# Optimization experiments

Measured on AMD Instinct MI355X. Metric: run time of the kernel, lower is better.

Reference implementation:

```python
import jax, jax.numpy as jnp
import numpy as np

D = 768
N_HEADS = 12
HEAD_DIM = 64
INNER = N_HEADS * HEAD_DIM
SCALE = HEAD_DIM ** -0.5
EPS = 1e-5


def setup_inputs() -> dict:
    key = jax.random.key(0)
    ks = jax.random.split(key, 7)
    s = 0.02
    return {
        "x": jax.random.normal(ks[0], (2, 2048, D), dtype=jnp.float32),
        "Wq": jax.random.normal(ks[1], (D, INNER), dtype=jnp.float32) * s,
        "Wk": jax.random.normal(ks[2], (D, INNER), dtype=jnp.float32) * s,
        "Wv": jax.random.normal(ks[3], (D, INNER), dtype=jnp.float32) * s,
        "Wo": jax.random.normal(ks[4], (INNER, D), dtype=jnp.float32) * s,
        "bo": jnp.zeros((D,), dtype=jnp.float32),
        "gamma": jnp.ones((D,), dtype=jnp.float32),
        "beta": jnp.zeros((D,), dtype=jnp.float32),
    }


def _layernorm(x, gamma, beta):
    mu = jnp.mean(x, axis=-1, keepdims=True)
    var = jnp.var(x, axis=-1, keepdims=True)
    return (x - mu) * jax.lax.rsqrt(var + EPS) * gamma + beta


def reference(x, Wq, Wk, Wv, Wo, bo, gamma, beta):
    b, n, _ = x.shape
    h = _layernorm(x, gamma, beta)
    # project and split heads: [b, n, inner] -> [b, h, n, d]
    def split(t):
        return t.reshape(b, n, N_HEADS, HEAD_DIM).transpose(0, 2, 1, 3)
    Q = split(h @ Wq)
    K = split(h @ Wk)
    V = split(h @ Wv)
    # NOTE: module applies softmax first, THEN multiplies probs by scale
    attn = jnp.einsum('bhid,bhjd->bhij', Q, K)
    attn = jax.nn.softmax(attn, axis=-1) * SCALE
    vals = jnp.einsum('bhij,bhjd->bhid', attn, V)
    vals = vals.transpose(0, 2, 1, 3).reshape(b, n, INNER)
    out = vals @ Wo + bo
    return x + out
```

## Files before the change

kernel.cpp:

```cpp
#include <hip/hip_runtime.h>
#include <stdint.h>

typedef __bf16 bf16;
typedef __bf16 bf16x8 __attribute__((ext_vector_type(8)));
typedef float  f32x4  __attribute__((ext_vector_type(4)));
typedef unsigned short u16x4 __attribute__((ext_vector_type(4)));
typedef unsigned int   u32x4v __attribute__((ext_vector_type(4)));

#define SEQ   2048
#define DM    768
#define NH    12
#define HD    64
#define ATT_SCALE 0.125f
#define LOG2E 1.44269504f
#define LN_EPS 1e-5f

__device__ __forceinline__ void gload16(const void* g, void* l) {
  __builtin_amdgcn_global_load_lds((const __attribute__((address_space(1))) void*)g,
                                   (__attribute__((address_space(3))) void*)l,
                                   16, 0, 0);
}

__global__ __launch_bounds__(256) void prep_kernel(
    const float* __restrict__ x, const float* __restrict__ gamma,
    const float* __restrict__ beta, bf16* __restrict__ h,
    const float* __restrict__ Wq, const float* __restrict__ Wk,
    const float* __restrict__ Wv, const float* __restrict__ Wo,
    bf16* __restrict__ Wqkvt, bf16* __restrict__ Wot)
{
  __shared__ float smem[32*33];
  int bid = blockIdx.x, t = threadIdx.x;
  if (bid < 4096) {
    const float* xr = x + (size_t)bid*DM;
    float v0 = xr[t], v1 = xr[t+256], v2 = xr[t+512];
    float s = v0+v1+v2;
    float q = v0*v0+v1*v1+v2*v2;
    #pragma unroll
    for (int m=32;m>=1;m>>=1){ s += __shfl_xor(s,m,64); q += __shfl_xor(q,m,64); }
    float* rs = smem; float* rq = smem+8;
    int w = t>>6;
    if ((t&63)==0){ rs[w]=s; rq[w]=q; }
    __syncthreads();
    float S = rs[0]+rs[1]+rs[2]+rs[3];
    float Q = rq[0]+rq[1]+rq[2]+rq[3];
    float mean = S*(1.0f/DM);
    float var  = Q*(1.0f/DM) - mean*mean;
    float rstd = rsqrtf(var + LN_EPS);
    bf16* hr = h + (size_t)bid*DM;
    hr[t]     = (bf16)((v0-mean)*rstd*gamma[t]     + beta[t]);
    hr[t+256] = (bf16)((v1-mean)*rstd*gamma[t+256] + beta[t+256]);
    hr[t+512] = (bf16)((v2-mean)*rstd*gamma[t+512] + beta[t+512]);
  } else {
    int tb = bid - 4096;
    int z = tb/576, rem = tb%576;
    int r0 = (rem/24)*32, c0 = (rem%24)*32;
    int tx = t&31, ty = t>>5;
    float (*tile)[33] = (float(*)[33])smem;
    const float* src = (z==0)?Wq:(z==1)?Wk:(z==2)?Wv:Wo;
    #pragma unroll
    for (int i=ty;i<32;i+=8) tile[i][tx] = src[(size_t)(r0+i)*DM + c0+tx];
    __syncthreads();
    bf16* dst = (z<3) ? (Wqkvt + (size_t)z*DM*DM) : Wot;
    #pragma unroll
    for (int i=ty;i<32;i+=8) dst[(size_t)(c0+i)*DM + r0+tx] = (bf16)tile[tx][i];
  }
}

template<int BM, int BN, int WM, int WN, int EPI>
__global__ __launch_bounds__(256) void gemm_bt(
    const bf16* __restrict__ A, const bf16* __restrict__ Bt, int K,
    bf16* __restrict__ qk, bf16* __restrict__ vt,
    float* __restrict__ out, const float* __restrict__ bo, const float* __restrict__ xres)
{
  constexpr int MF = BM/(WM*16);
  constexpr int NF = BN/(WN*16);
  constexpr int GL = BM/64 + BN/64;
  __shared__ bf16 As[3][BM][32];
  __shared__ bf16 Bs[3][BN][32];
  int tid = threadIdx.x, w = tid>>6, la = tid&63;
  int bn = blockIdx.x, bm = blockIdx.y;
  int wm = w / WN, wn = w % WN;
  int g = la>>4, li = la&15;
  int sr = la>>2, sc = (la&3)*8;
  f32x4 acc[MF][NF] = {};
  const int KT = K/32;

  auto stage = [&](int kt, int bb) {
    int k0 = kt*32;
    #pragma unroll
    for (int i=0;i<BM/64;i++){ int r0 = i*64 + w*16;
      gload16(A + ((size_t)(bm*BM + r0 + sr))*K + k0 + sc, &As[bb][r0][0]); }
    #pragma unroll
    for (int i=0;i<BN/64;i++){ int r0 = i*64 + w*16;
      gload16(Bt + ((size_t)(bn*BN + r0 + sr))*K + k0 + sc, &Bs[bb][r0][0]); }
  };

  stage(0,0); stage(1,1);
  asm volatile("s_waitcnt vmcnt(%0)" :: "n"(GL) : "memory");
  __builtin_amdgcn_s_barrier();
  __builtin_amdgcn_sched_barrier(0);

  for (int kt=0; kt<KT; ++kt) {
    int bb = kt%3;
    if (kt+2 < KT) stage(kt+2, (kt+2)%3);
    bf16x8 af[MF], bfr[NF];
    #pragma unroll
    for (int i=0;i<MF;i++) af[i]  = *(const bf16x8*)&As[bb][wm*(BM/WM)+i*16+li][g*8];
    #pragma unroll
    for (int j=0;j<NF;j++) bfr[j] = *(const bf16x8*)&Bs[bb][wn*(BN/WN)+j*16+li][g*8];
    __builtin_amdgcn_s_setprio(1);
    #pragma unroll
    for (int i=0;i<MF;i++)
      #pragma unroll
      for (int j=0;j<NF;j++)
        acc[i][j] = __builtin_amdgcn_mfma_f32_16x16x32_bf16(af[i], bfr[j], acc[i][j], 0,0,0);
    __builtin_amdgcn_s_setprio(0);
    if (kt+1 < KT) {
      if (kt+2 < KT) asm volatile("s_waitcnt vmcnt(%0)" :: "n"(GL) : "memory");
      else           asm volatile("s_waitcnt vmcnt(0)" ::: "memory");
      __builtin_amdgcn_s_barrier();
      __builtin_amdgcn_sched_barrier(0);
    }
  }

  #pragma unroll
  for (int i=0;i<MF;i++){
    int row0 = bm*BM + wm*(BM/WM) + i*16 + g*4;
    #pragma unroll
    for (int j=0;j<NF;j++){
      int col = bn*BN + wn*(BN/WN) + j*16 + li;
      if (EPI==0){
        if (col < 1536) {
          float qs = (col < 768) ? LOG2E : 1.0f;
          #pragma unroll
          for (int r=0;r<4;r++) qk[(size_t)(row0+r)*1536 + col] = (bf16)(acc[i][j][r]*qs);
        } else {
          int cv = col - 1536; int hh = cv>>6, dd = cv&63;
          int b_ = row0>>11,  n0 = row0&2047;
          u16x4 u;
          #pragma unroll
          for (int r=0;r<4;r++){ bf16 bv = (bf16)acc[i][j][r];
            u[r] = __builtin_bit_cast(unsigned short, bv); }
          *reinterpret_cast<u16x4*>(vt + ((size_t)((b_*NH+hh)*HD+dd))*SEQ + n0) = u;
        }
      } else {
        float bb2 = bo[col];
        #pragma unroll
        for (int r=0;r<4;r++){ size_t idx = (size_t)(row0+r)*DM + col;
          out[idx] = acc[i][j][r] + bb2 + xres[idx]; }
      }
    }
  }
}

__global__ __launch_bounds__(256) void attn_kernel(
    const bf16* __restrict__ QK, const bf16* __restrict__ Vt, bf16* __restrict__ vals)
{
  __shared__ bf16 Ks[3][64][64];
  __shared__ bf16 Vs[3][64][64];
  int tid=threadIdx.x, w=tid>>6, la=tid&63;
  int id = blockIdx.x;
  int xcd = id & 7, idx = id >> 3;
  int bh  = xcd*3 + (idx>>5);
  int qt  = idx & 31;
  int b = bh/NH, hh = bh%NH;
  int g=la>>4, li=la&15;
  int lr=la>>3;
  int lx=li&7;
  int lcs=((la&7)^lr)*8;
  size_t qrow0=(size_t)b*SEQ + qt*64;

  bf16x8 qf[2];
  {
    const bf16* qp = QK + (qrow0 + w*16 + li)*1536 + hh*64;
    qf[0] = *(const bf16x8*)(qp + g*8);
    qf[1] = *(const bf16x8*)(qp + 32 + g*8);
  }

  const bf16* Kbase = QK + (size_t)b*SEQ*1536 + 768 + hh*64;
  const bf16* Vbase = Vt + (size_t)(b*NH+hh)*HD*SEQ;

  auto stage = [&](int tt, int bb) {
    int j0 = tt*64;
    #pragma unroll
    for (int i=0;i<2;i++){ int c=i*4+w;
      gload16(Kbase + (size_t)(j0 + c*8 + lr)*1536 + lcs, &Ks[bb][c*8][0]);
      gload16(Vbase + (size_t)(c*8 + lr)*SEQ + j0 + lcs,  &Vs[bb][c*8][0]); }
  };

  stage(0,0); stage(1,1);
  asm volatile("s_waitcnt vmcnt(4)" ::: "memory");
  __builtin_amdgcn_s_barrier();
  __builtin_amdgcn_sched_barrier(0);

  f32x4 o[4] = {};
  float lp[4] = {0.f,0.f,0.f,0.f};

  for (int t=0;t<32;t++){
    int bb = t%3;
    if (t+2 < 32) stage(t+2, (t+2)%3);
    f32x4 s[4] = {};
    #pragma unroll
    for (int kk=0;kk<2;kk++){
      bf16x8 kf[4];
      #pragma unroll
      for (int nf=0;nf<4;nf++){
        int row = nf*16+li;
        kf[nf] = *(const bf16x8*)((const char*)&Ks[bb][0][0] + row*128 + (((kk*4+g)^lx)<<4));
      }
      __builtin_amdgcn_s_setprio(1);
      #pragma unroll
      for (int nf=0;nf<4;nf++)
        s[nf] = __builtin_amdgcn_mfma_f32_16x16x32_bf16(kf[nf], qf[kk], s[nf], 0,0,0);
      __builtin_amdgcn_s_setprio(0);
    }
    float p[4][4];
    #pragma unroll
    for (int nf=0;nf<4;nf++){
      #pragma unroll
      for (int r=0;r<4;r++){
        p[nf][r] = __builtin_amdgcn_exp2f(s[nf][r]);
        lp[nf] += p[nf][r];
      }
    }
    bf16x8 pa[2];
    #pragma unroll
    for (int ks=0;ks<2;ks++){
      unsigned int c00,c01,c10,c11;
      asm("v_cvt_pk_bf16_f32 %0, %1, %2" : "=v"(c00) : "v"(p[2*ks  ][0]), "v"(p[2*ks  ][1]));
      asm("v_cvt_pk_bf16_f32 %0, %1, %2" : "=v"(c01) : "v"(p[2*ks  ][2]), "v"(p[2*ks  ][3]));
      asm("v_cvt_pk_bf16_f32 %0, %1, %2" : "=v"(c10) : "v"(p[2*ks+1][0]), "v"(p[2*ks+1][1]));
      asm("v_cvt_pk_bf16_f32 %0, %1, %2" : "=v"(c11) : "v"(p[2*ks+1][2]), "v"(p[2*ks+1][3]));
      asm("v_permlane32_swap_b32 %0, %1" : "+v"(c00), "+v"(c10));
      asm("v_permlane32_swap_b32 %0, %1" : "+v"(c01), "+v"(c11));
      asm("v_permlane16_swap_b32 %0, %1" : "+v"(c00), "+v"(c10));
      asm("v_permlane16_swap_b32 %0, %1" : "+v"(c01), "+v"(c11));
      u32x4v cc = {c00, c01, c10, c11};
      pa[ks] = __builtin_bit_cast(bf16x8, cc);
    }
    #pragma unroll
    for (int ks=0;ks<2;ks++){
      bf16x8 vb[4];
      #pragma unroll
      for (int df=0;df<4;df++){
        int row = df*16+li;
        vb[df] = *(const bf16x8*)((const char*)&Vs[bb][0][0] + row*128 + (((ks*4+g)^lx)<<4));
      }
      __builtin_amdgcn_s_setprio(1);
      #pragma unroll
      for (int df=0;df<4;df++)
        o[df] = __builtin_amdgcn_mfma_f32_16x16x32_bf16(vb[df], pa[ks], o[df], 0,0,0);
      __builtin_amdgcn_s_setprio(0);
    }
    if (t+1 < 32) {
      if (t+2 < 32) asm volatile("s_waitcnt vmcnt(4)" ::: "memory");
      else          asm volatile("s_waitcnt vmcnt(0)" ::: "memory");
      __builtin_amdgcn_s_barrier();
      __builtin_amdgcn_sched_barrier(0);
    }
  }
  float lsum = lp[0]+lp[1]+lp[2]+lp[3];
  lsum += __shfl_xor(lsum, 16, 64);
  lsum += __shfl_xor(lsum, 32, 64);
  float fac = ATT_SCALE / lsum;
  bf16* vrow = vals + (qrow0 + w*16 + li)*DM + hh*64;
  #pragma unroll
  for (int df=0;df<4;df++){
    u16x4 u;
    #pragma unroll
    for (int r=0;r<4;r++){
      bf16 bv = (bf16)(o[df][r] * fac);
      u[r] = __builtin_bit_cast(unsigned short, bv);
    }
    *reinterpret_cast<u16x4*>(vrow + df*16 + g*4) = u;
  }
}

extern "C" void kernel_launch(void* const* d_in, const int* in_sizes, int n_in,
                              void* d_out, int out_size, void* d_ws, size_t ws_size,
                              hipStream_t stream)
{
  const float* x     = (const float*)d_in[0];
  const float* Wq    = (const float*)d_in[1];
  const float* Wk    = (const float*)d_in[2];
  const float* Wv    = (const float*)d_in[3];
  const float* Wo    = (const float*)d_in[4];
  const float* bo    = (const float*)d_in[5];
  const float* gamma = (const float*)d_in[6];
  const float* beta  = (const float*)d_in[7];
  float* out = (float*)d_out;
  char* ws = (char*)d_ws;

  bf16* h     = (bf16*)(ws + 0);
  bf16* vals  = (bf16*)(ws + 0);
  bf16* Wqkvt = (bf16*)(ws + 6291456);
  bf16* Wot   = (bf16*)(ws + 9830400);
  bf16* QKb   = (bf16*)(ws + 11010048);
  bf16* Vt    = (bf16*)(ws + 23592960);
  (void)ws_size; (void)in_sizes; (void)n_in; (void)out_size;

  prep_kernel<<<dim3(6400), dim3(256), 0, stream>>>(
      x, gamma, beta, h, Wq, Wk, Wv, Wo, Wqkvt, Wot);
  gemm_bt<128,128,2,2,0><<<dim3(18,32), dim3(256), 0, stream>>>(
      h, Wqkvt, DM, QKb, Vt, nullptr, nullptr, nullptr);
  attn_kernel<<<dim3(768), dim3(256), 0, stream>>>(QKb, Vt, vals);
  gemm_bt<64,64,2,2,1><<<dim3(12,64), dim3(256), 0, stream>>>(
      vals, Wot, DM, nullptr, nullptr, out, bo, x);
}
```

Measured before the change: 103.4 us.

## Halve attention waves, give each wave two query tiles, compute row sums via MFMA

Each attention block now runs 2 waves instead of 4, and each wave handles 32 query rows (two 16-row halves). This reuses every K and V fragment loaded from LDS across two MFMA calls, cutting LDS read traffic per FLOP. The softmax row-sum is now taken by an extra MFMA against a ones vector, which removes the per-element VALU adds and the cross-lane shuffles. In exchange, each wave holds roughly twice the registers and each block has fewer waves to hide latency. Global-to-LDS staging is spread over fewer threads, so the waitcnt thresholds are adjusted to match.

```diff
diff --git a/kernel.cpp b/kernel.cpp
--- a/kernel.cpp
+++ b/kernel.cpp
@@ -153,7 +153,7 @@
   }
 }
 
-__global__ __launch_bounds__(256) void attn_kernel(
+__global__ __launch_bounds__(128) void attn_kernel(
     const bf16* __restrict__ QK, const bf16* __restrict__ Vt, bf16* __restrict__ vals)
 {
   __shared__ bf16 Ks[3][64][64];
@@ -170,11 +170,19 @@
   int lcs=((la&7)^lr)*8;
   size_t qrow0=(size_t)b*SEQ + qt*64;
 
-  bf16x8 qf[2];
+  bf16x8 qf[2][2];
+  #pragma unroll
+  for (int qh=0;qh<2;qh++){
+    const bf16* qp = QK + (qrow0 + w*32 + qh*16 + li)*1536 + hh*64;
+    qf[0][qh] = *(const bf16x8*)(qp + g*8);
+    qf[1][qh] = *(const bf16x8*)(qp + 32 + g*8);
+  }
+
+  bf16x8 onef;
   {
-    const bf16* qp = QK + (qrow0 + w*16 + li)*1536 + hh*64;
-    qf[0] = *(const bf16x8*)(qp + g*8);
-    qf[1] = *(const bf16x8*)(qp + 32 + g*8);
+    unsigned int one2 = 0x3F803F80u;
+    u32x4v oc = {one2, one2, one2, one2};
+    onef = __builtin_bit_cast(bf16x8, oc);
   }
 
   const bf16* Kbase = QK + (size_t)b*SEQ*1536 + 768 + hh*64;
@@ -183,23 +191,23 @@
   auto stage = [&](int tt, int bb) {
     int j0 = tt*64;
     #pragma unroll
-    for (int i=0;i<2;i++){ int c=i*4+w;
+    for (int i=0;i<4;i++){ int c=i*2+w;
       gload16(Kbase + (size_t)(j0 + c*8 + lr)*1536 + lcs, &Ks[bb][c*8][0]);
       gload16(Vbase + (size_t)(c*8 + lr)*SEQ + j0 + lcs,  &Vs[bb][c*8][0]); }
   };
 
   stage(0,0); stage(1,1);
-  asm volatile("s_waitcnt vmcnt(4)" ::: "memory");
+  asm volatile("s_waitcnt vmcnt(8)" ::: "memory");
   __builtin_amdgcn_s_barrier();
   __builtin_amdgcn_sched_barrier(0);
 
-  f32x4 o[4] = {};
-  float lp[4] = {0.f,0.f,0.f,0.f};
+  f32x4 o[2][4] = {};
+  f32x4 ol[2] = {};
 
   for (int t=0;t<32;t++){
     int bb = t%3;
     if (t+2 < 32) stage(t+2, (t+2)%3);
-    f32x4 s[4] = {};
+    f32x4 s[2][4] = {};
     #pragma unroll
     for (int kk=0;kk<2;kk++){
       bf16x8 kf[4];
@@ -210,33 +218,35 @@
       }
       __builtin_amdgcn_s_setprio(1);
       #pragma unroll
+      for (int nf=0;nf<4;nf++){
+        s[0][nf] = __builtin_amdgcn_mfma_f32_16x16x32_bf16(kf[nf], qf[kk][0], s[0][nf], 0,0,0);
+        s[1][nf] = __builtin_amdgcn_mfma_f32_16x16x32_bf16(kf[nf], qf[kk][1], s[1][nf], 0,0,0);
+      }
+      __builtin_amdgcn_s_setprio(0);
+    }
+    bf16x8 pa[2][2];
+    #pragma unroll
+    for (int qh=0;qh<2;qh++){
+      float p[4][4];
+      #pragma unroll
       for (int nf=0;nf<4;nf++)
-        s[nf] = __builtin_amdgcn_mfma_f32_16x16x32_bf16(kf[nf], qf[kk], s[nf], 0,0,0);
-      __builtin_amdgcn_s_setprio(0);
-    }
-    float p[4][4];
-    #pragma unroll
-    for (int nf=0;nf<4;nf++){
-      #pragma unroll
-      for (int r=0;r<4;r++){
-        p[nf][r] = __builtin_amdgcn_exp2f(s[nf][r]);
-        lp[nf] += p[nf][r];
-      }
-    }
-    bf16x8 pa[2];
-    #pragma unroll
-    for (int ks=0;ks<2;ks++){
-      unsigned int c00,c01,c10,c11;
-      asm("v_cvt_pk_bf16_f32 %0, %1, %2" : "=v"(c00) : "v"(p[2*ks  ][0]), "v"(p[2*ks  ][1]));
-      asm("v_cvt_pk_bf16_f32 %0, %1, %2" : "=v"(c01) : "v"(p[2*ks  ][2]), "v"(p[2*ks  ][3]));
-      asm("v_cvt_pk_bf16_f32 %0, %1, %2" : "=v"(c10) : "v"(p[2*ks+1][0]), "v"(p[2*ks+1][1]));
-      asm("v_cvt_pk_bf16_f32 %0, %1, %2" : "=v"(c11) : "v"(p[2*ks+1][2]), "v"(p[2*ks+1][3]));
-      asm("v_permlane32_swap_b32 %0, %1" : "+v"(c00), "+v"(c10));
-      asm("v_permlane32_swap_b32 %0, %1" : "+v"(c01), "+v"(c11));
-      asm("v_permlane16_swap_b32 %0, %1" : "+v"(c00), "+v"(c10));
-      asm("v_permlane16_swap_b32 %0, %1" : "+v"(c01), "+v"(c11));
-      u32x4v cc = {c00, c01, c10, c11};
-      pa[ks] = __builtin_bit_cast(bf16x8, cc);
+        #pragma unroll
+        for (int r=0;r<4;r++)
+          p[nf][r] = __builtin_amdgcn_exp2f(s[qh][nf][r]);
+      #pragma unroll
+      for (int ks=0;ks<2;ks++){
+        unsigned int c00,c01,c10,c11;
+        asm("v_cvt_pk_bf16_f32 %0, %1, %2" : "=v"(c00) : "v"(p[2*ks  ][0]), "v"(p[2*ks  ][1]));
+        asm("v_cvt_pk_bf16_f32 %0, %1, %2" : "=v"(c01) : "v"(p[2*ks  ][2]), "v"(p[2*ks  ][3]));
+        asm("v_cvt_pk_bf16_f32 %0, %1, %2" : "=v"(c10) : "v"(p[2*ks+1][0]), "v"(p[2*ks+1][1]));
+        asm("v_cvt_pk_bf16_f32 %0, %1, %2" : "=v"(c11) : "v"(p[2*ks+1][2]), "v"(p[2*ks+1][3]));
+        asm("v_permlane32_swap_b32 %0, %1" : "+v"(c00), "+v"(c10));
+        asm("v_permlane32_swap_b32 %0, %1" : "+v"(c01), "+v"(c11));
+        asm("v_permlane16_swap_b32 %0, %1" : "+v"(c00), "+v"(c10));
+        asm("v_permlane16_swap_b32 %0, %1" : "+v"(c01), "+v"(c11));
+        u32x4v cc = {c00, c01, c10, c11};
+        pa[qh][ks] = __builtin_bit_cast(bf16x8, cc);
+      }
     }
     #pragma unroll
     for (int ks=0;ks<2;ks++){
@@ -248,31 +258,35 @@
       }
       __builtin_amdgcn_s_setprio(1);
       #pragma unroll
-      for (int df=0;df<4;df++)
-        o[df] = __builtin_amdgcn_mfma_f32_16x16x32_bf16(vb[df], pa[ks], o[df], 0,0,0);
+      for (int qh=0;qh<2;qh++){
+        #pragma unroll
+        for (int df=0;df<4;df++)
+          o[qh][df] = __builtin_amdgcn_mfma_f32_16x16x32_bf16(vb[df], pa[qh][ks], o[qh][df], 0,0,0);
+        ol[qh] = __builtin_amdgcn_mfma_f32_16x16x32_bf16(onef, pa[qh][ks], ol[qh], 0,0,0);
+      }
       __builtin_amdgcn_s_setprio(0);
     }
     if (t+1 < 32) {
-      if (t+2 < 32) asm volatile("s_waitcnt vmcnt(4)" ::: "memory");
+      if (t+2 < 32) asm volatile("s_waitcnt vmcnt(8)" ::: "memory");
       else          asm volatile("s_waitcnt vmcnt(0)" ::: "memory");
       __builtin_amdgcn_s_barrier();
       __builtin_amdgcn_sched_barrier(0);
     }
   }
-  float lsum = lp[0]+lp[1]+lp[2]+lp[3];
-  lsum += __shfl_xor(lsum, 16, 64);
-  lsum += __shfl_xor(lsum, 32, 64);
-  float fac = ATT_SCALE / lsum;
-  bf16* vrow = vals + (qrow0 + w*16 + li)*DM + hh*64;
   #pragma unroll
-  for (int df=0;df<4;df++){
-    u16x4 u;
-    #pragma unroll
-    for (int r=0;r<4;r++){
-      bf16 bv = (bf16)(o[df][r] * fac);
-      u[r] = __builtin_bit_cast(unsigned short, bv);
-    }
-    *reinterpret_cast<u16x4*>(vrow + df*16 + g*4) = u;
+  for (int qh=0;qh<2;qh++){
+    float fac = ATT_SCALE / ol[qh][0];
+    bf16* vrow = vals + (qrow0 + w*32 + qh*16 + li)*DM + hh*64;
+    #pragma unroll
+    for (int df=0;df<4;df++){
+      u16x4 u;
+      #pragma unroll
+      for (int r=0;r<4;r++){
+        bf16 bv = (bf16)(o[qh][df][r] * fac);
+        u[r] = __builtin_bit_cast(unsigned short, bv);
+      }
+      *reinterpret_cast<u16x4*>(vrow + df*16 + g*4) = u;
+    }
   }
 }
 
@@ -303,7 +317,7 @@
       x, gamma, beta, h, Wq, Wk, Wv, Wo, Wqkvt, Wot);
   gemm_bt<128,128,2,2,0><<<dim3(18,32), dim3(256), 0, stream>>>(
       h, Wqkvt, DM, QKb, Vt, nullptr, nullptr, nullptr);
-  attn_kernel<<<dim3(768), dim3(256), 0, stream>>>(QKb, Vt, vals);
+  attn_kernel<<<dim3(768), dim3(128), 0, stream>>>(QKb, Vt, vals);
   gemm_bt<64,64,2,2,1><<<dim3(12,64), dim3(256), 0, stream>>>(
       vals, Wot, DM, nullptr, nullptr, out, bo, x);
 }
```

Result: slower. 114.0 us (+10.2%).

## Split attention KV range across two wave groups and merge partials in LDS

Applied to the files above, without the earlier changes.

Doubles the attention block to 512 threads, with each half of the waves processing half of the key/value sequence for the same 64 query rows. The second half writes its unnormalized bf16 partial outputs and row sums to LDS, and the first half combines them before normalizing and storing. This halves the serial KV loop length per wave and adds waves per block. In exchange the pipeline drops from triple to double buffering with a full vmcnt(0) wait each iteration, and the partial output is rounded to bf16 before the merge, which costs some precision.

```diff
diff --git a/kernel.cpp b/kernel.cpp
--- a/kernel.cpp
+++ b/kernel.cpp
@@ -153,15 +153,19 @@
   }
 }
 
-__global__ __launch_bounds__(256) void attn_kernel(
-    const bf16* __restrict__ QK, const bf16* __restrict__ Vt, bf16* __restrict__ vals)
+__global__ __launch_bounds__(512) void attn_kernel(
+    const bf16* __restrict__ QK, const bf16* __restrict__ Vt,
+    bf16* __restrict__ vals)
 {
-  __shared__ bf16 Ks[3][64][64];
-  __shared__ bf16 Vs[3][64][64];
+  __shared__ bf16 Ks[2][2][64][64];
+  __shared__ bf16 Vs[2][2][64][64];
+  __shared__ bf16 Om[4][16][64];
+  __shared__ float lm[64];
   int tid=threadIdx.x, w=tid>>6, la=tid&63;
+  int half = w>>2, wl = w&3;
   int id = blockIdx.x;
   int xcd = id & 7, idx = id >> 3;
-  int bh  = xcd*3 + (idx>>5);
+  int bh  = xcd*3 + idx/32;
   int qt  = idx & 31;
   int b = bh/NH, hh = bh%NH;
   int g=la>>4, li=la&15;
@@ -169,10 +173,11 @@
   int lx=li&7;
   int lcs=((la&7)^lr)*8;
   size_t qrow0=(size_t)b*SEQ + qt*64;
+  int kv0 = half*1024;
 
   bf16x8 qf[2];
   {
-    const bf16* qp = QK + (qrow0 + w*16 + li)*1536 + hh*64;
+    const bf16* qp = QK + (qrow0 + wl*16 + li)*1536 + hh*64;
     qf[0] = *(const bf16x8*)(qp + g*8);
     qf[1] = *(const bf16x8*)(qp + 32 + g*8);
   }
@@ -180,25 +185,25 @@
   const bf16* Kbase = QK + (size_t)b*SEQ*1536 + 768 + hh*64;
   const bf16* Vbase = Vt + (size_t)(b*NH+hh)*HD*SEQ;
 
-  auto stage = [&](int tt, int bb) {
-    int j0 = tt*64;
-    #pragma unroll
-    for (int i=0;i<2;i++){ int c=i*4+w;
-      gload16(Kbase + (size_t)(j0 + c*8 + lr)*1536 + lcs, &Ks[bb][c*8][0]);
-      gload16(Vbase + (size_t)(c*8 + lr)*SEQ + j0 + lcs,  &Vs[bb][c*8][0]); }
+  auto stage = [&](int tt, int bbuf) {
+    int j0 = kv0 + tt*64;
+    #pragma unroll
+    for (int i=0;i<2;i++){ int c=i*4+wl;
+      gload16(Kbase + (size_t)(j0 + c*8 + lr)*1536 + lcs, &Ks[half][bbuf][c*8][0]);
+      gload16(Vbase + (size_t)(c*8 + lr)*SEQ + j0 + lcs,  &Vs[half][bbuf][c*8][0]); }
   };
 
-  stage(0,0); stage(1,1);
-  asm volatile("s_waitcnt vmcnt(4)" ::: "memory");
+  stage(0,0);
+  asm volatile("s_waitcnt vmcnt(0)" ::: "memory");
   __builtin_amdgcn_s_barrier();
   __builtin_amdgcn_sched_barrier(0);
 
   f32x4 o[4] = {};
   float lp[4] = {0.f,0.f,0.f,0.f};
 
-  for (int t=0;t<32;t++){
-    int bb = t%3;
-    if (t+2 < 32) stage(t+2, (t+2)%3);
+  for (int t=0;t<16;t++){
+    int bb = t&1;
+    if (t+1 < 16) stage(t+1, bb^1);
     f32x4 s[4] = {};
     #pragma unroll
     for (int kk=0;kk<2;kk++){
@@ -206,7 +211,7 @@
       #pragma unroll
       for (int nf=0;nf<4;nf++){
         int row = nf*16+li;
-        kf[nf] = *(const bf16x8*)((const char*)&Ks[bb][0][0] + row*128 + (((kk*4+g)^lx)<<4));
+        kf[nf] = *(const bf16x8*)((const char*)&Ks[half][bb][0][0] + row*128 + (((kk*4+g)^lx)<<4));
       }
       __builtin_amdgcn_s_setprio(1);
       #pragma unroll
@@ -244,7 +249,7 @@
       #pragma unroll
       for (int df=0;df<4;df++){
         int row = df*16+li;
-        vb[df] = *(const bf16x8*)((const char*)&Vs[bb][0][0] + row*128 + (((ks*4+g)^lx)<<4));
+        vb[df] = *(const bf16x8*)((const char*)&Vs[half][bb][0][0] + row*128 + (((ks*4+g)^lx)<<4));
       }
       __builtin_amdgcn_s_setprio(1);
       #pragma unroll
@@ -252,9 +257,8 @@
         o[df] = __builtin_amdgcn_mfma_f32_16x16x32_bf16(vb[df], pa[ks], o[df], 0,0,0);
       __builtin_amdgcn_s_setprio(0);
     }
-    if (t+1 < 32) {
-      if (t+2 < 32) asm volatile("s_waitcnt vmcnt(4)" ::: "memory");
-      else          asm volatile("s_waitcnt vmcnt(0)" ::: "memory");
+    if (t+1 < 16) {
+      asm volatile("s_waitcnt vmcnt(0)" ::: "memory");
       __builtin_amdgcn_s_barrier();
       __builtin_amdgcn_sched_barrier(0);
     }
@@ -262,17 +266,39 @@
   float lsum = lp[0]+lp[1]+lp[2]+lp[3];
   lsum += __shfl_xor(lsum, 16, 64);
   lsum += __shfl_xor(lsum, 32, 64);
-  float fac = ATT_SCALE / lsum;
-  bf16* vrow = vals + (qrow0 + w*16 + li)*DM + hh*64;
-  #pragma unroll
-  for (int df=0;df<4;df++){
-    u16x4 u;
-    #pragma unroll
-    for (int r=0;r<4;r++){
-      bf16 bv = (bf16)(o[df][r] * fac);
-      u[r] = __builtin_bit_cast(unsigned short, bv);
-    }
-    *reinterpret_cast<u16x4*>(vrow + df*16 + g*4) = u;
+  int swz = (li&7)<<4;
+  if (half==1){
+    char* om = (char*)&Om[wl][0][0];
+    #pragma unroll
+    for (int df=0;df<4;df++){
+      u16x4 u;
+      #pragma unroll
+      for (int r=0;r<4;r++){
+        bf16 bv = (bf16)o[df][r];
+        u[r] = __builtin_bit_cast(unsigned short, bv);
+      }
+      *reinterpret_cast<u16x4*>(om + li*128 + ((df*32 + g*8) ^ swz)) = u;
+    }
+    if (g==0) lm[wl*16+li] = lsum;
+  }
+  __syncthreads();
+  if (half==0){
+    const char* om = (const char*)&Om[wl][0][0];
+    float ltot = lsum + lm[wl*16+li];
+    float fac = ATT_SCALE / ltot;
+    bf16* vrow = vals + (qrow0 + wl*16 + li)*DM + hh*64;
+    #pragma unroll
+    for (int df=0;df<4;df++){
+      u16x4 pu = *reinterpret_cast<const u16x4*>(om + li*128 + ((df*32 + g*8) ^ swz));
+      u16x4 u;
+      #pragma unroll
+      for (int r=0;r<4;r++){
+        float pv = (float)__builtin_bit_cast(bf16, pu[r]);
+        bf16 bv = (bf16)((o[df][r] + pv) * fac);
+        u[r] = __builtin_bit_cast(unsigned short, bv);
+      }
+      *reinterpret_cast<u16x4*>(vrow + df*16 + g*4) = u;
+    }
   }
 }
 
@@ -303,7 +329,7 @@
       x, gamma, beta, h, Wq, Wk, Wv, Wo, Wqkvt, Wot);
   gemm_bt<128,128,2,2,0><<<dim3(18,32), dim3(256), 0, stream>>>(
       h, Wqkvt, DM, QKb, Vt, nullptr, nullptr, nullptr);
-  attn_kernel<<<dim3(768), dim3(256), 0, stream>>>(QKb, Vt, vals);
+  attn_kernel<<<dim3(768), dim3(512), 0, stream>>>(QKb, Vt, vals);
   gemm_bt<64,64,2,2,1><<<dim3(12,64), dim3(256), 0, stream>>>(
       vals, Wot, DM, nullptr, nullptr, out, bo, x);
 }
```

After: 104.1 us. Within noise of the previous version (+0.6%).
